# Performance work log

Hardware: AMD Instinct MI355X
Metric: run time of the kernel (lower is better)

The kernel has to match this reference:

```python
import jax, jax.numpy as jnp
import numpy as np

ROUTE_SCALE = 2.5
TOP_K = 2
N_EXPERTS = 16


def setup_inputs() -> dict:
    key = jax.random.key(0)
    ks = jax.random.split(key, 8)
    B, T, D, I, E = 2, 1024, 768, 384, N_EXPERTS
    s = 0.02
    return {
        "x": jax.random.normal(ks[0], (B, T, D), dtype=jnp.float32),
        "gate_w": jax.random.normal(ks[1], (E, D), dtype=jnp.float32) * s,
        "sg_w": jax.random.normal(ks[2], (I, D), dtype=jnp.float32) * s,
        "su_w": jax.random.normal(ks[3], (I, D), dtype=jnp.float32) * s,
        "sd_w": jax.random.normal(ks[4], (D, I), dtype=jnp.float32) * s,
        "rg_w": jax.random.normal(ks[5], (E, I, D), dtype=jnp.float32) * s,
        "ru_w": jax.random.normal(ks[6], (E, I, D), dtype=jnp.float32) * s,
        "rd_w": jax.random.normal(ks[7], (E, D, I), dtype=jnp.float32) * s,
    }


def _moe_forward(x, gate_w, sg_w, su_w, sd_w, rg_w, ru_w, rd_w):
    B, T, D = x.shape
    flat = x.reshape(-1, D)  # (N, D), N = B*T

    # ---- shared expert (SwiGLU FFN) ----
    g = flat @ sg_w.T
    u = flat @ su_w.T
    shared_out = (jax.nn.silu(g) * u) @ sd_w.T  # (N, D)

    # ---- gate: softmax(fp32) -> top-k -> renormalize ----
    logits = (flat @ gate_w.T) * ROUTE_SCALE  # (N, E)
    scores = jax.nn.softmax(logits.astype(jnp.float32), axis=-1)
    topk_w, topk_i = jax.lax.top_k(scores, TOP_K)  # (N, K)
    topk_w = topk_w / jnp.sum(topk_w, axis=-1, keepdims=True)
    topk_w = topk_w.astype(x.dtype)

    # aux load-balancing loss
    one_hot = jax.nn.one_hot(topk_i, N_EXPERTS, dtype=jnp.float32)  # (N, K, E)
    mask = one_hot.sum(axis=1)  # (N, E)
    f = mask.mean(axis=0)
    p = scores.mean(axis=0)
    aux_loss = jnp.sum(f * p) * N_EXPERTS

    # combine weights per (token, expert): sum_k w_k * [idx_k == e]
    combine = jnp.einsum("nk,nke->ne", topk_w, one_hot.astype(x.dtype))  # (N, E)

    # ---- routed experts as batched (grouped) SwiGLU GEMMs ----
    rg = jnp.einsum("nd,eid->nei", flat, rg_w)  # (N, E, I)
    ru = jnp.einsum("nd,eid->nei", flat, ru_w)
    rh = jax.nn.silu(rg) * ru  # (N, E, I)
    eo = jnp.einsum("nei,edi->ned", rh, rd_w)  # (N, E, D)
    routed_out = jnp.einsum("ned,ne->nd", eo, combine)  # (N, D)

    out = (shared_out + routed_out).reshape(B, T, D)
    return out, aux_loss


def reference(x, gate_w, sg_w, su_w, sd_w, rg_w, ru_w, rd_w):
    return _moe_forward(x, gate_w, sg_w, su_w, sd_w, rg_w, ru_w, rd_w)
```

## Files before the change

### kernel.cpp

```cpp
#include <hip/hip_runtime.h>
#include <math.h>

#define NTOK 2048
#define DDIM 768
#define IDIM 384
#define NEXP 16
#define ECAP 2048
#define HSHARED (NEXP * ECAP)
#define GBLK (NTOK / 4)

#define MT 64
#define NSHT2 32
#define NRT2 80
#define NW2 ((NSHT2 + NRT2) * 6)
#define CH2 (NW2 / 8)
#define KH 384

#define ZBLK4 384
#define XBLK4 192
#define W1BLK4 (72 * 17)
#define WDBLK4 (36 * 17)
#define CZBLK (ZBLK4 + XBLK4 + W1BLK4 + WDBLK4)

typedef __attribute__((ext_vector_type(8))) short short8;
typedef __attribute__((ext_vector_type(4))) float f32x4;

__device__ __forceinline__ unsigned short f2bf(float f) {
    unsigned int u = __float_as_uint(f);
    unsigned int r = (u + 0x7fffu + ((u >> 16) & 1u)) >> 16;
    return (unsigned short)r;
}

__device__ __forceinline__ void gload16(const void* g, void* l) {
    __builtin_amdgcn_global_load_lds(
        (const __attribute__((address_space(1))) void*)g,
        (__attribute__((address_space(3))) void*)l, 16, 0, 0);
}

#define WS_XB   1048576u
#define WS_W1F  4194304u
#define WS_WDF  24248320u
#define WS_H    34275328u

__global__ __launch_bounds__(256) void gate_kernel(
    const float* __restrict__ x, const float* __restrict__ gate_w,
    int* __restrict__ topk_i, float* __restrict__ topk_w,
    float* __restrict__ p_partial) {
    __shared__ float p_blk[16];
    int tid = threadIdx.x;
    if (tid < 16) p_blk[tid] = 0.f;
    __syncthreads();

    int wave = tid >> 6, lane = tid & 63;
    int n = blockIdx.x * 4 + wave;
    int e = lane >> 2, q = lane & 3;
    const float4* xr = (const float4*)(x + (size_t)n * DDIM);
    const float4* wr = (const float4*)(gate_w + (size_t)e * DDIM);
    float s = 0.f;
    #pragma unroll 4
    for (int k = q * 48; k < q * 48 + 48; ++k) {
        float4 a = xr[k], b = wr[k];
        s += a.x * b.x + a.y * b.y + a.z * b.z + a.w * b.w;
    }
    s += __shfl_xor(s, 1);
    s += __shfl_xor(s, 2);
    float logit = s * 2.5f;

    float m = logit;
    #pragma unroll
    for (int mask = 4; mask < 64; mask <<= 1)
        m = fmaxf(m, __shfl_xor(m, mask));
    float ex = __expf(logit - m);
    float sum = ex;
    #pragma unroll
    for (int mask = 4; mask < 64; mask <<= 1)
        sum += __shfl_xor(sum, mask);
    float sc = ex / sum;

    float v = sc; int idx = e;
    #pragma unroll
    for (int mask = 4; mask < 64; mask <<= 1) {
        float ov = __shfl_xor(v, mask);
        int   oi = __shfl_xor(idx, mask);
        if (ov > v || (ov == v && oi < idx)) { v = ov; idx = oi; }
    }
    float b0 = v; int i0 = idx;
    v = (e == i0) ? -1.f : sc; idx = e;
    #pragma unroll
    for (int mask = 4; mask < 64; mask <<= 1) {
        float ov = __shfl_xor(v, mask);
        int   oi = __shfl_xor(idx, mask);
        if (ov > v || (ov == v && oi < idx)) { v = ov; idx = oi; }
    }
    float b1 = v; int i1 = idx;
    float rs = 1.f / (b0 + b1);

    if (lane == 0) {
        topk_i[n * 2] = i0; topk_i[n * 2 + 1] = i1;
        topk_w[n * 2] = b0 * rs; topk_w[n * 2 + 1] = b1 * rs;
    }
    if (q == 0) atomicAdd(&p_blk[e], sc);
    __syncthreads();
    if (tid < 16) p_partial[blockIdx.x * 16 + tid] = p_blk[tid];
}

__global__ __launch_bounds__(256) void convzero_kernel(
    const float* __restrict__ x,
    const float* __restrict__ rgw, const float* __restrict__ ruw,
    const float* __restrict__ sgw, const float* __restrict__ suw,
    const float* __restrict__ rdw, const float* __restrict__ sdw,
    float4* __restrict__ out4,
    unsigned short* __restrict__ xb, unsigned short* __restrict__ w1f,
    unsigned short* __restrict__ wdf) {
    int b = blockIdx.x, tid = threadIdx.x;

    if (b < ZBLK4) {
        float4 z = make_float4(0.f, 0.f, 0.f, 0.f);
        float4* dst = out4 + b * 1024 + tid;
        #pragma unroll
        for (int j = 0; j < 4; ++j) dst[j * 256] = z;
        return;
    }
    b -= ZBLK4;

    if (b < XBLK4) {
        #pragma unroll
        for (int j = 0; j < 4; ++j) {
            int i = b * 1024 + j * 256 + tid;
            const float* s = x + (size_t)i * 8;
            float4 v0 = *(const float4*)s, v1 = *(const float4*)(s + 4);
            short8 o;
            o[0]=f2bf(v0.x); o[1]=f2bf(v0.y); o[2]=f2bf(v0.z); o[3]=f2bf(v0.w);
            o[4]=f2bf(v1.x); o[5]=f2bf(v1.y); o[6]=f2bf(v1.z); o[7]=f2bf(v1.w);
            *(short8*)(xb + (size_t)i * 8) = o;
        }
        return;
    }
    b -= XBLK4;

    if (b < W1BLK4) {
        int E = b / 72, bx = b % 72;
        const float* gsrc = (E == 16) ? sgw : rgw + (size_t)E * (IDIM * DDIM);
        const float* usrc = (E == 16) ? suw : ruw + (size_t)E * (IDIM * DDIM);
        unsigned short* wbase = w1f + (size_t)E * (DDIM * DDIM);
        #pragma unroll
        for (int j = 0; j < 4; ++j) {
            int i = bx * 1024 + j * 256 + tid;
            int lane = i & 63;
            int fi = i >> 6;
            int ks = fi % 24, rg = fi / 24;
            int b16 = rg >> 1, gu = rg & 1;
            const float* s = (gu ? usrc : gsrc)
              + (size_t)(b16 * 16 + (lane & 15)) * DDIM + ks * 32 + (lane >> 4) * 8;
            float4 v0 = *(const float4*)s, v1 = *(const float4*)(s + 4);
            short8 o;
            o[0]=f2bf(v0.x); o[1]=f2bf(v0.y); o[2]=f2bf(v0.z); o[3]=f2bf(v0.w);
            o[4]=f2bf(v1.x); o[5]=f2bf(v1.y); o[6]=f2bf(v1.z); o[7]=f2bf(v1.w);
            *(short8*)(wbase + (size_t)i * 8) = o;
        }
        return;
    }
    b -= W1BLK4;

    {
        int E = b / 36, bx = b % 36;
        const float* src = (E == 16) ? sdw : rdw + (size_t)E * (DDIM * IDIM);
        unsigned short* wbase = wdf + (size_t)E * (DDIM * IDIM);
        #pragma unroll
        for (int j = 0; j < 4; ++j) {
            int i = bx * 1024 + j * 256 + tid;
            int lane = i & 63;
            int fi = i >> 6;
            int ks = fi % 12, cg = fi / 12;
            const float* s = src
              + (size_t)(cg * 16 + (lane & 15)) * IDIM + ks * 32 + (lane >> 4) * 8;
            float4 v0 = *(const float4*)s, v1 = *(const float4*)(s + 4);
            short8 o;
            o[0]=f2bf(v0.x); o[1]=f2bf(v0.y); o[2]=f2bf(v0.z); o[3]=f2bf(v0.w);
            o[4]=f2bf(v1.x); o[5]=f2bf(v1.y); o[6]=f2bf(v1.z); o[7]=f2bf(v1.w);
            *(short8*)(wbase + (size_t)i * 8) = o;
        }
    }
}

__global__ __launch_bounds__(256) void route_kernel(
    const int* __restrict__ topk_i, const float* __restrict__ topk_w,
    const float* __restrict__ p_partial,
    int* __restrict__ counts, int* __restrict__ perm_t, float* __restrict__ perm_w,
    float* __restrict__ out_aux) {
    __shared__ float s_p[256];
    __shared__ float s_psum[16];
    __shared__ int s_cnt[16];
    __shared__ int s_cur[16];
    int tid = threadIdx.x;
    {
        int e = tid & 15, g = tid >> 4;
        float acc = 0.f;
        for (int b = g; b < GBLK; b += 16) acc += p_partial[b * 16 + e];
        s_p[tid] = acc;
    }
    if (tid < 16) { s_cnt[tid] = 0; s_cur[tid] = 0; }
    __syncthreads();
    if (tid < 16) {
        float a = 0.f;
        #pragma unroll
        for (int g = 0; g < 16; ++g) a += s_p[g * 16 + tid];
        s_psum[tid] = a;
    }
    for (int n = tid; n < NTOK; n += 256) {
        atomicAdd(&s_cnt[topk_i[n * 2]], 1);
        atomicAdd(&s_cnt[topk_i[n * 2 + 1]], 1);
    }
    __syncthreads();
    if (tid < 16) counts[tid] = s_cnt[tid];
    if (tid == 0) {
        float a = 0.f;
        for (int e = 0; e < 16; ++e) a += (float)s_cnt[e] * s_psum[e];
        out_aux[0] = a * 16.f / ((float)NTOK * (float)NTOK);
    }
    for (int n = tid; n < NTOK; n += 256) {
        #pragma unroll
        for (int k = 0; k < 2; ++k) {
            int e = topk_i[n * 2 + k];
            int pos = atomicAdd(&s_cur[e], 1);
            perm_t[e * ECAP + pos] = n;
            perm_w[e * ECAP + pos] = topk_w[n * 2 + k];
        }
    }
}

__device__ __forceinline__ void swz_decode(int lid, int& bx, int& y) {
    int wid = (lid & 7) * CH2 + (lid >> 3);
    bx = wid / 6;
    y = wid - bx * 6;
}

__device__ __forceinline__ bool tile_decode(const int* __restrict__ counts,
                                            int r, int& e, int& t, int& cnt) {
    int acc = 0;
    for (int ee = 0; ee < NEXP; ++ee) {
        int c = counts[ee];
        int tiles = (c + 63) >> 6;
        if (r < acc + tiles) { e = ee; t = r - acc; cnt = c; return true; }
        acc += tiles;
    }
    return false;
}

__global__ __launch_bounds__(256, 3) void p1_kernel(
    const unsigned short* __restrict__ xb, const unsigned short* __restrict__ w1f,
    const int* __restrict__ counts, const int* __restrict__ perm_t,
    unsigned short* __restrict__ h) {
    __shared__ unsigned short xs[48 * 512];
    __shared__ int s_tok[MT];

    int tid = threadIdx.x;
    int bx, y;
    swz_decode(blockIdx.x, bx, y);
    int e, hbase;
    if (bx < NSHT2) {
        e = 16;
        hbase = HSHARED + bx * MT;
        if (tid < MT) s_tok[tid] = bx * MT + tid;
    } else {
        int t, cnt;
        if (!tile_decode(counts, bx - NSHT2, e, t, cnt)) return;
        hbase = e * ECAP + t * MT;
        if (tid < MT) {
            int slot = t * MT + tid;
            s_tok[tid] = (slot < cnt) ? perm_t[e * ECAP + slot] : 0;
        }
    }
    __syncthreads();

    int lane = tid & 63, wave = tid >> 6;
    int lr = lane & 15, kg8 = (lane >> 4) * 8, jrow = (lane >> 4) * 4;

    const unsigned short* gsrc = xb + (size_t)s_tok[wave * 16 + lr] * DDIM + kg8;

    const unsigned short* pg = w1f + ((((size_t)e * 48 + (y * 8 + wave * 2    )) * 24) * 64 + lane) * 8;
    const unsigned short* pu = w1f + ((((size_t)e * 48 + (y * 8 + wave * 2 + 1)) * 24) * 64 + lane) * 8;

    f32x4 ag0 = (f32x4)0.f, ag1 = (f32x4)0.f, ag2 = (f32x4)0.f, ag3 = (f32x4)0.f;
    f32x4 au0 = (f32x4)0.f, au1 = (f32x4)0.f, au2 = (f32x4)0.f, au3 = (f32x4)0.f;

    #pragma unroll
    for (int half = 0; half < 2; ++half) {
        if (half) __syncthreads();
        #pragma unroll
        for (int c = 0; c < 12; ++c)
            gload16(gsrc + half * KH + c * 32, &xs[(wave * 12 + c) * 512]);
        __syncthreads();

        for (int ks = 0; ks < 12; ++ks) {
            int ksg = half * 12 + ks;
            short8 bg = *(const short8*)(pg + (size_t)ksg * 512);
            short8 bu = *(const short8*)(pu + (size_t)ksg * 512);
            short8 a0 = *(const short8*)(xs + (     ks) * 512 + lane * 8);
            short8 a1 = *(const short8*)(xs + (12 + ks) * 512 + lane * 8);
            short8 a2 = *(const short8*)(xs + (24 + ks) * 512 + lane * 8);
            short8 a3 = *(const short8*)(xs + (36 + ks) * 512 + lane * 8);
            ag0 = __builtin_amdgcn_mfma_f32_16x16x32_bf16(a0, bg, ag0, 0, 0, 0);
            au0 = __builtin_amdgcn_mfma_f32_16x16x32_bf16(a0, bu, au0, 0, 0, 0);
            ag1 = __builtin_amdgcn_mfma_f32_16x16x32_bf16(a1, bg, ag1, 0, 0, 0);
            au1 = __builtin_amdgcn_mfma_f32_16x16x32_bf16(a1, bu, au1, 0, 0, 0);
            ag2 = __builtin_amdgcn_mfma_f32_16x16x32_bf16(a2, bg, ag2, 0, 0, 0);
            au2 = __builtin_amdgcn_mfma_f32_16x16x32_bf16(a2, bu, au2, 0, 0, 0);
            ag3 = __builtin_amdgcn_mfma_f32_16x16x32_bf16(a3, bg, ag3, 0, 0, 0);
            au3 = __builtin_amdgcn_mfma_f32_16x16x32_bf16(a3, bu, au3, 0, 0, 0);
        }
    }

    int colg = y * 64 + wave * 16 + lr;
    #pragma unroll
    for (int mf = 0; mf < 4; ++mf) {
        f32x4 g4 = (mf == 0) ? ag0 : (mf == 1) ? ag1 : (mf == 2) ? ag2 : ag3;
        f32x4 u4 = (mf == 0) ? au0 : (mf == 1) ? au1 : (mf == 2) ? au2 : au3;
        #pragma unroll
        for (int j = 0; j < 4; ++j) {
            int tl = mf * 16 + jrow + j;
            float g = g4[j], u = u4[j];
            float hv = g / (1.f + __expf(-g)) * u;
            h[(size_t)(hbase + tl) * IDIM + colg] = f2bf(hv);
        }
    }
}

__global__ __launch_bounds__(256, 3) void p2_kernel(
    const unsigned short* __restrict__ h, const unsigned short* __restrict__ wdf,
    const int* __restrict__ counts,
    const int* __restrict__ perm_t, const float* __restrict__ perm_w,
    float* __restrict__ out) {
    __shared__ unsigned short hs[48 * 512];
    __shared__ int   s_tok[MT];
    __shared__ float s_w[MT];

    int tid = threadIdx.x;
    int bx, y;
    swz_decode(blockIdx.x, bx, y);
    int e, hbase;
    if (bx < NSHT2) {
        e = 16;
        hbase = HSHARED + bx * MT;
        if (tid < MT) { s_tok[tid] = bx * MT + tid; s_w[tid] = 1.f; }
    } else {
        int t, cnt;
        if (!tile_decode(counts, bx - NSHT2, e, t, cnt)) return;
        hbase = e * ECAP + t * MT;
        if (tid < MT) {
            int slot = t * MT + tid;
            bool v = slot < cnt;
            s_tok[tid] = v ? perm_t[e * ECAP + slot] : 0;
            s_w[tid]   = v ? perm_w[e * ECAP + slot] : 0.f;
        }
    }
    __syncthreads();

    int lane = tid & 63, wave = tid >> 6;
    int lr = lane & 15, kg8 = (lane >> 4) * 8, jrow = (lane >> 4) * 4;

    const unsigned short* gsrc = h + (size_t)(hbase + wave * 16 + lr) * IDIM + kg8;
    #pragma unroll
    for (int c = 0; c < 12; ++c)
        gload16(gsrc + c * 32, &hs[(wave * 12 + c) * 512]);
    __syncthreads();

    const unsigned short* p0 = wdf + ((((size_t)e * 48 + (y * 8 + wave * 2    )) * 12) * 64 + lane) * 8;
    const unsigned short* p1 = wdf + ((((size_t)e * 48 + (y * 8 + wave * 2 + 1)) * 12) * 64 + lane) * 8;

    f32x4 c00 = (f32x4)0.f, c01 = (f32x4)0.f, c02 = (f32x4)0.f, c03 = (f32x4)0.f;
    f32x4 c10 = (f32x4)0.f, c11 = (f32x4)0.f, c12 = (f32x4)0.f, c13 = (f32x4)0.f;
    for (int ks = 0; ks < 12; ++ks) {
        short8 b0 = *(const short8*)(p0 + (size_t)ks * 512);
        short8 b1 = *(const short8*)(p1 + (size_t)ks * 512);
        short8 a0 = *(const short8*)(hs + (     ks) * 512 + lane * 8);
        short8 a1 = *(const short8*)(hs + (12 + ks) * 512 + lane * 8);
        short8 a2 = *(const short8*)(hs + (24 + ks) * 512 + lane * 8);
        short8 a3 = *(const short8*)(hs + (36 + ks) * 512 + lane * 8);
        c00 = __builtin_amdgcn_mfma_f32_16x16x32_bf16(a0, b0, c00, 0, 0, 0);
        c10 = __builtin_amdgcn_mfma_f32_16x16x32_bf16(a0, b1, c10, 0, 0, 0);
        c01 = __builtin_amdgcn_mfma_f32_16x16x32_bf16(a1, b0, c01, 0, 0, 0);
        c11 = __builtin_amdgcn_mfma_f32_16x16x32_bf16(a1, b1, c11, 0, 0, 0);
        c02 = __builtin_amdgcn_mfma_f32_16x16x32_bf16(a2, b0, c02, 0, 0, 0);
        c12 = __builtin_amdgcn_mfma_f32_16x16x32_bf16(a2, b1, c12, 0, 0, 0);
        c03 = __builtin_amdgcn_mfma_f32_16x16x32_bf16(a3, b0, c03, 0, 0, 0);
        c13 = __builtin_amdgcn_mfma_f32_16x16x32_bf16(a3, b1, c13, 0, 0, 0);
    }

    int col0 = y * 128 + wave * 32 + lr;
    #pragma unroll
    for (int mf = 0; mf < 4; ++mf) {
        f32x4 v0 = (mf == 0) ? c00 : (mf == 1) ? c01 : (mf == 2) ? c02 : c03;
        f32x4 v1 = (mf == 0) ? c10 : (mf == 1) ? c11 : (mf == 2) ? c12 : c13;
        #pragma unroll
        for (int j = 0; j < 4; ++j) {
            int tl = mf * 16 + jrow + j;
            float w = s_w[tl];
            if (w == 0.f) continue;
            float* orow = out + (size_t)s_tok[tl] * DDIM;
            atomicAdd(orow + col0,      w * v0[j]);
            atomicAdd(orow + col0 + 16, w * v1[j]);
        }
    }
}

extern "C" void kernel_launch(void* const* d_in, const int* in_sizes, int n_in,
                              void* d_out, int out_size, void* d_ws, size_t ws_size,
                              hipStream_t stream) {
    const float* x      = (const float*)d_in[0];
    const float* gate_w = (const float*)d_in[1];
    const float* sg_w   = (const float*)d_in[2];
    const float* su_w   = (const float*)d_in[3];
    const float* sd_w   = (const float*)d_in[4];
    const float* rg_w   = (const float*)d_in[5];
    const float* ru_w   = (const float*)d_in[6];
    const float* rd_w   = (const float*)d_in[7];
    float* out = (float*)d_out;

    char* ws = (char*)d_ws;
    int*   counts    = (int*)(ws + 0);
    int*   perm_t    = (int*)(ws + 1024);
    float* perm_w    = (float*)(ws + 132096);
    float* p_partial = (float*)(ws + 263168);
    int*   topk_i    = (int*)(ws + 295936);
    float* topk_w    = (float*)(ws + 312320);
    unsigned short* xb  = (unsigned short*)(ws + WS_XB);
    unsigned short* w1f = (unsigned short*)(ws + WS_W1F);
    unsigned short* wdf = (unsigned short*)(ws + WS_WDF);
    unsigned short* hbuf= (unsigned short*)(ws + WS_H);

    gate_kernel<<<GBLK, 256, 0, stream>>>(x, gate_w, topk_i, topk_w, p_partial);

    convzero_kernel<<<CZBLK, 256, 0, stream>>>(
        x, rg_w, ru_w, sg_w, su_w, rd_w, sd_w,
        (float4*)out, xb, w1f, wdf);

    route_kernel<<<1, 256, 0, stream>>>(topk_i, topk_w, p_partial,
                                        counts, perm_t, perm_w,
                                        out + (size_t)NTOK * DDIM);

    p1_kernel<<<NW2, 256, 0, stream>>>(xb, w1f, counts, perm_t, hbuf);

    p2_kernel<<<NW2, 256, 0, stream>>>(hbuf, wdf, counts, perm_t, perm_w, out);
}
```

Measured before the change: 101.8 us.

## Fuse routing into conversion kernel, stage weight repack via LDS, shrink GEMM LDS chunks

Merges the single-block route kernel into the conversion/zeroing kernel as block 0, removing one launch and its serialization. Weight repacking to the MFMA fragment layout now reads rows coalesced into a padded LDS buffer and writes fragments out, instead of doing strided scattered global reads. The p1 and p2 GEMM kernels load their activation tile in smaller K chunks, halving LDS use so occupancy can rise from 3 to 4 blocks per CU, at the cost of more barriers.

```diff
diff --git a/kernel.cpp b/kernel.cpp
--- a/kernel.cpp
+++ b/kernel.cpp
@@ -14,13 +14,12 @@
 #define NRT2 80
 #define NW2 ((NSHT2 + NRT2) * 6)
 #define CH2 (NW2 / 8)
-#define KH 384
-
-#define ZBLK4 384
-#define XBLK4 192
-#define W1BLK4 (72 * 17)
-#define WDBLK4 (36 * 17)
-#define CZBLK (ZBLK4 + XBLK4 + W1BLK4 + WDBLK4)
+
+#define CR_Z0 1
+#define CR_X0 (CR_Z0 + 384)
+#define CR_W10 (CR_X0 + 192)
+#define CR_WD0 (CR_W10 + 816)
+#define CR_END (CR_WD0 + 816)
 
 typedef __attribute__((ext_vector_type(8))) short short8;
 typedef __attribute__((ext_vector_type(4))) float f32x4;
@@ -104,29 +103,76 @@
     if (tid < 16) p_partial[blockIdx.x * 16 + tid] = p_blk[tid];
 }
 
-__global__ __launch_bounds__(256) void convzero_kernel(
+__global__ __launch_bounds__(256) void convroute_kernel(
     const float* __restrict__ x,
     const float* __restrict__ rgw, const float* __restrict__ ruw,
     const float* __restrict__ sgw, const float* __restrict__ suw,
     const float* __restrict__ rdw, const float* __restrict__ sdw,
     float4* __restrict__ out4,
     unsigned short* __restrict__ xb, unsigned short* __restrict__ w1f,
-    unsigned short* __restrict__ wdf) {
+    unsigned short* __restrict__ wdf,
+    const int* __restrict__ topk_i, const float* __restrict__ topk_w,
+    const float* __restrict__ p_partial,
+    int* __restrict__ counts, int* __restrict__ perm_t, float* __restrict__ perm_w,
+    float* __restrict__ out_aux) {
+    __shared__ unsigned short sbuf[16 * 780];
     int b = blockIdx.x, tid = threadIdx.x;
 
-    if (b < ZBLK4) {
+    if (b == 0) {
+        float* s_p    = (float*)sbuf;
+        float* s_psum = s_p + 256;
+        int*   s_cnt  = (int*)(s_psum + 16);
+        int*   s_cur  = s_cnt + 16;
+        {
+            int e = tid & 15, g = tid >> 4;
+            float acc = 0.f;
+            for (int bb = g; bb < GBLK; bb += 16) acc += p_partial[bb * 16 + e];
+            s_p[tid] = acc;
+        }
+        if (tid < 16) { s_cnt[tid] = 0; s_cur[tid] = 0; }
+        __syncthreads();
+        if (tid < 16) {
+            float a = 0.f;
+            #pragma unroll
+            for (int g = 0; g < 16; ++g) a += s_p[g * 16 + tid];
+            s_psum[tid] = a;
+        }
+        for (int n = tid; n < NTOK; n += 256) {
+            atomicAdd(&s_cnt[topk_i[n * 2]], 1);
+            atomicAdd(&s_cnt[topk_i[n * 2 + 1]], 1);
+        }
+        __syncthreads();
+        if (tid < 16) counts[tid] = s_cnt[tid];
+        if (tid == 0) {
+            float a = 0.f;
+            for (int e = 0; e < 16; ++e) a += (float)s_cnt[e] * s_psum[e];
+            out_aux[0] = a * 16.f / ((float)NTOK * (float)NTOK);
+        }
+        for (int n = tid; n < NTOK; n += 256) {
+            #pragma unroll
+            for (int k = 0; k < 2; ++k) {
+                int e = topk_i[n * 2 + k];
+                int pos = atomicAdd(&s_cur[e], 1);
+                perm_t[e * ECAP + pos] = n;
+                perm_w[e * ECAP + pos] = topk_w[n * 2 + k];
+            }
+        }
+        return;
+    }
+
+    if (b < CR_X0) {
         float4 z = make_float4(0.f, 0.f, 0.f, 0.f);
-        float4* dst = out4 + b * 1024 + tid;
+        float4* dst = out4 + (b - CR_Z0) * 1024 + tid;
         #pragma unroll
         for (int j = 0; j < 4; ++j) dst[j * 256] = z;
         return;
     }
-    b -= ZBLK4;
-
-    if (b < XBLK4) {
+
+    if (b < CR_W10) {
+        int bb = b - CR_X0;
         #pragma unroll
         for (int j = 0; j < 4; ++j) {
-            int i = b * 1024 + j * 256 + tid;
+            int i = bb * 1024 + j * 256 + tid;
             const float* s = x + (size_t)i * 8;
             float4 v0 = *(const float4*)s, v1 = *(const float4*)(s + 4);
             short8 o;
@@ -136,95 +182,56 @@
         }
         return;
     }
-    b -= XBLK4;
-
-    if (b < W1BLK4) {
-        int E = b / 72, bx = b % 72;
-        const float* gsrc = (E == 16) ? sgw : rgw + (size_t)E * (IDIM * DDIM);
-        const float* usrc = (E == 16) ? suw : ruw + (size_t)E * (IDIM * DDIM);
-        unsigned short* wbase = w1f + (size_t)E * (DDIM * DDIM);
-        #pragma unroll
-        for (int j = 0; j < 4; ++j) {
-            int i = bx * 1024 + j * 256 + tid;
-            int lane = i & 63;
-            int fi = i >> 6;
-            int ks = fi % 24, rg = fi / 24;
-            int b16 = rg >> 1, gu = rg & 1;
-            const float* s = (gu ? usrc : gsrc)
-              + (size_t)(b16 * 16 + (lane & 15)) * DDIM + ks * 32 + (lane >> 4) * 8;
-            float4 v0 = *(const float4*)s, v1 = *(const float4*)(s + 4);
-            short8 o;
-            o[0]=f2bf(v0.x); o[1]=f2bf(v0.y); o[2]=f2bf(v0.z); o[3]=f2bf(v0.w);
-            o[4]=f2bf(v1.x); o[5]=f2bf(v1.y); o[6]=f2bf(v1.z); o[7]=f2bf(v1.w);
-            *(short8*)(wbase + (size_t)i * 8) = o;
+
+    if (b < CR_WD0) {
+        int bb = b - CR_W10;
+        int E = bb / 48, rg = bb % 48;
+        const float* gsrc_ = (E == 16) ? sgw : rgw + (size_t)E * (IDIM * DDIM);
+        const float* usrc_ = (E == 16) ? suw : ruw + (size_t)E * (IDIM * DDIM);
+        const float* src = ((rg & 1) ? usrc_ : gsrc_) + (size_t)(rg >> 1) * 16 * DDIM;
+        #pragma unroll
+        for (int i = 0; i < 12; ++i) {
+            int idx = i * 256 + tid;
+            int r = idx / 192, c4 = idx - r * 192;
+            float4 v = ((const float4*)(src + (size_t)r * DDIM))[c4];
+            ushort4 o4;
+            o4.x = f2bf(v.x); o4.y = f2bf(v.y); o4.z = f2bf(v.z); o4.w = f2bf(v.w);
+            *(ushort4*)(sbuf + r * 780 + c4 * 4) = o4;
+        }
+        __syncthreads();
+        unsigned short* wbase = w1f + (size_t)E * (DDIM * DDIM) + (size_t)rg * 24 * 512;
+        #pragma unroll
+        for (int c = 0; c < 6; ++c) {
+            int cc = c * 256 + tid;
+            int ks = cc >> 6, l = cc & 63;
+            short8 v8 = *(const short8*)(sbuf + (l & 15) * 780 + ks * 32 + (l >> 4) * 8);
+            *(short8*)(wbase + (size_t)(ks * 64 + l) * 8) = v8;
         }
         return;
     }
-    b -= W1BLK4;
 
     {
-        int E = b / 36, bx = b % 36;
-        const float* src = (E == 16) ? sdw : rdw + (size_t)E * (DDIM * IDIM);
-        unsigned short* wbase = wdf + (size_t)E * (DDIM * IDIM);
-        #pragma unroll
-        for (int j = 0; j < 4; ++j) {
-            int i = bx * 1024 + j * 256 + tid;
-            int lane = i & 63;
-            int fi = i >> 6;
-            int ks = fi % 12, cg = fi / 12;
-            const float* s = src
-              + (size_t)(cg * 16 + (lane & 15)) * IDIM + ks * 32 + (lane >> 4) * 8;
-            float4 v0 = *(const float4*)s, v1 = *(const float4*)(s + 4);
-            short8 o;
-            o[0]=f2bf(v0.x); o[1]=f2bf(v0.y); o[2]=f2bf(v0.z); o[3]=f2bf(v0.w);
-            o[4]=f2bf(v1.x); o[5]=f2bf(v1.y); o[6]=f2bf(v1.z); o[7]=f2bf(v1.w);
-            *(short8*)(wbase + (size_t)i * 8) = o;
-        }
-    }
-}
-
-__global__ __launch_bounds__(256) void route_kernel(
-    const int* __restrict__ topk_i, const float* __restrict__ topk_w,
-    const float* __restrict__ p_partial,
-    int* __restrict__ counts, int* __restrict__ perm_t, float* __restrict__ perm_w,
-    float* __restrict__ out_aux) {
-    __shared__ float s_p[256];
-    __shared__ float s_psum[16];
-    __shared__ int s_cnt[16];
-    __shared__ int s_cur[16];
-    int tid = threadIdx.x;
-    {
-        int e = tid & 15, g = tid >> 4;
-        float acc = 0.f;
-        for (int b = g; b < GBLK; b += 16) acc += p_partial[b * 16 + e];
-        s_p[tid] = acc;
-    }
-    if (tid < 16) { s_cnt[tid] = 0; s_cur[tid] = 0; }
-    __syncthreads();
-    if (tid < 16) {
-        float a = 0.f;
-        #pragma unroll
-        for (int g = 0; g < 16; ++g) a += s_p[g * 16 + tid];
-        s_psum[tid] = a;
-    }
-    for (int n = tid; n < NTOK; n += 256) {
-        atomicAdd(&s_cnt[topk_i[n * 2]], 1);
-        atomicAdd(&s_cnt[topk_i[n * 2 + 1]], 1);
-    }
-    __syncthreads();
-    if (tid < 16) counts[tid] = s_cnt[tid];
-    if (tid == 0) {
-        float a = 0.f;
-        for (int e = 0; e < 16; ++e) a += (float)s_cnt[e] * s_psum[e];
-        out_aux[0] = a * 16.f / ((float)NTOK * (float)NTOK);
-    }
-    for (int n = tid; n < NTOK; n += 256) {
-        #pragma unroll
-        for (int k = 0; k < 2; ++k) {
-            int e = topk_i[n * 2 + k];
-            int pos = atomicAdd(&s_cur[e], 1);
-            perm_t[e * ECAP + pos] = n;
-            perm_w[e * ECAP + pos] = topk_w[n * 2 + k];
+        int bb = b - CR_WD0;
+        int E = bb / 48, cg = bb % 48;
+        const float* src = ((E == 16) ? sdw : rdw + (size_t)E * (DDIM * IDIM))
+                         + (size_t)cg * 16 * IDIM;
+        #pragma unroll
+        for (int i = 0; i < 6; ++i) {
+            int idx = i * 256 + tid;
+            int r = idx / 96, c4 = idx - r * 96;
+            float4 v = ((const float4*)(src + (size_t)r * IDIM))[c4];
+            ushort4 o4;
+            o4.x = f2bf(v.x); o4.y = f2bf(v.y); o4.z = f2bf(v.z); o4.w = f2bf(v.w);
+            *(ushort4*)(sbuf + r * 390 + c4 * 4) = o4;
+        }
+        __syncthreads();
+        unsigned short* wbase = wdf + (size_t)E * (DDIM * IDIM) + (size_t)cg * 12 * 512;
+        #pragma unroll
+        for (int c = 0; c < 3; ++c) {
+            int cc = c * 256 + tid;
+            int ks = cc >> 6, l = cc & 63;
+            short8 v8 = *(const short8*)(sbuf + (l & 15) * 390 + ks * 32 + (l >> 4) * 8);
+            *(short8*)(wbase + (size_t)(ks * 64 + l) * 8) = v8;
         }
     }
 }
@@ -247,11 +254,11 @@
     return false;
 }
 
-__global__ __launch_bounds__(256, 3) void p1_kernel(
+__global__ __launch_bounds__(256, 4) void p1_kernel(
     const unsigned short* __restrict__ xb, const unsigned short* __restrict__ w1f,
     const int* __restrict__ counts, const int* __restrict__ perm_t,
     unsigned short* __restrict__ h) {
-    __shared__ unsigned short xs[48 * 512];
+    __shared__ unsigned short xs[24 * 512];
     __shared__ int s_tok[MT];
 
     int tid = threadIdx.x;
@@ -284,22 +291,22 @@
     f32x4 ag0 = (f32x4)0.f, ag1 = (f32x4)0.f, ag2 = (f32x4)0.f, ag3 = (f32x4)0.f;
     f32x4 au0 = (f32x4)0.f, au1 = (f32x4)0.f, au2 = (f32x4)0.f, au3 = (f32x4)0.f;
 
-    #pragma unroll
-    for (int half = 0; half < 2; ++half) {
-        if (half) __syncthreads();
-        #pragma unroll
-        for (int c = 0; c < 12; ++c)
-            gload16(gsrc + half * KH + c * 32, &xs[(wave * 12 + c) * 512]);
-        __syncthreads();
-
-        for (int ks = 0; ks < 12; ++ks) {
-            int ksg = half * 12 + ks;
+    for (int ch = 0; ch < 4; ++ch) {
+        if (ch) __syncthreads();
+        #pragma unroll
+        for (int c = 0; c < 6; ++c)
+            gload16(gsrc + (ch * 6 + c) * 32, &xs[(wave * 6 + c) * 512]);
+        __syncthreads();
+
+        #pragma unroll
+        for (int ksl = 0; ksl < 6; ++ksl) {
+            int ksg = ch * 6 + ksl;
             short8 bg = *(const short8*)(pg + (size_t)ksg * 512);
             short8 bu = *(const short8*)(pu + (size_t)ksg * 512);
-            short8 a0 = *(const short8*)(xs + (     ks) * 512 + lane * 8);
-            short8 a1 = *(const short8*)(xs + (12 + ks) * 512 + lane * 8);
-            short8 a2 = *(const short8*)(xs + (24 + ks) * 512 + lane * 8);
-            short8 a3 = *(const short8*)(xs + (36 + ks) * 512 + lane * 8);
+            short8 a0 = *(const short8*)(xs + (     ksl) * 512 + lane * 8);
+            short8 a1 = *(const short8*)(xs + ( 6 + ksl) * 512 + lane * 8);
+            short8 a2 = *(const short8*)(xs + (12 + ksl) * 512 + lane * 8);
+            short8 a3 = *(const short8*)(xs + (18 + ksl) * 512 + lane * 8);
             ag0 = __builtin_amdgcn_mfma_f32_16x16x32_bf16(a0, bg, ag0, 0, 0, 0);
             au0 = __builtin_amdgcn_mfma_f32_16x16x32_bf16(a0, bu, au0, 0, 0, 0);
             ag1 = __builtin_amdgcn_mfma_f32_16x16x32_bf16(a1, bg, ag1, 0, 0, 0);
@@ -326,12 +333,12 @@
     }
 }
 
-__global__ __launch_bounds__(256, 3) void p2_kernel(
+__global__ __launch_bounds__(256, 4) void p2_kernel(
     const unsigned short* __restrict__ h, const unsigned short* __restrict__ wdf,
     const int* __restrict__ counts,
     const int* __restrict__ perm_t, const float* __restrict__ perm_w,
     float* __restrict__ out) {
-    __shared__ unsigned short hs[48 * 512];
+    __shared__ unsigned short hs[24 * 512];
     __shared__ int   s_tok[MT];
     __shared__ float s_w[MT];
 
@@ -360,31 +367,38 @@
     int lr = lane & 15, kg8 = (lane >> 4) * 8, jrow = (lane >> 4) * 4;
 
     const unsigned short* gsrc = h + (size_t)(hbase + wave * 16 + lr) * IDIM + kg8;
-    #pragma unroll
-    for (int c = 0; c < 12; ++c)
-        gload16(gsrc + c * 32, &hs[(wave * 12 + c) * 512]);
-    __syncthreads();
 
     const unsigned short* p0 = wdf + ((((size_t)e * 48 + (y * 8 + wave * 2    )) * 12) * 64 + lane) * 8;
     const unsigned short* p1 = wdf + ((((size_t)e * 48 + (y * 8 + wave * 2 + 1)) * 12) * 64 + lane) * 8;
 
     f32x4 c00 = (f32x4)0.f, c01 = (f32x4)0.f, c02 = (f32x4)0.f, c03 = (f32x4)0.f;
     f32x4 c10 = (f32x4)0.f, c11 = (f32x4)0.f, c12 = (f32x4)0.f, c13 = (f32x4)0.f;
-    for (int ks = 0; ks < 12; ++ks) {
-        short8 b0 = *(const short8*)(p0 + (size_t)ks * 512);
-        short8 b1 = *(const short8*)(p1 + (size_t)ks * 512);
-        short8 a0 = *(const short8*)(hs + (     ks) * 512 + lane * 8);
-        short8 a1 = *(const short8*)(hs + (12 + ks) * 512 + lane * 8);
-        short8 a2 = *(const short8*)(hs + (24 + ks) * 512 + lane * 8);
-        short8 a3 = *(const short8*)(hs + (36 + ks) * 512 + lane * 8);
-        c00 = __builtin_amdgcn_mfma_f32_16x16x32_bf16(a0, b0, c00, 0, 0, 0);
-        c10 = __builtin_amdgcn_mfma_f32_16x16x32_bf16(a0, b1, c10, 0, 0, 0);
-        c01 = __builtin_amdgcn_mfma_f32_16x16x32_bf16(a1, b0, c01, 0, 0, 0);
-        c11 = __builtin_amdgcn_mfma_f32_16x16x32_bf16(a1, b1, c11, 0, 0, 0);
-        c02 = __builtin_amdgcn_mfma_f32_16x16x32_bf16(a2, b0, c02, 0, 0, 0);
-        c12 = __builtin_amdgcn_mfma_f32_16x16x32_bf16(a2, b1, c12, 0, 0, 0);
-        c03 = __builtin_amdgcn_mfma_f32_16x16x32_bf16(a3, b0, c03, 0, 0, 0);
-        c13 = __builtin_amdgcn_mfma_f32_16x16x32_bf16(a3, b1, c13, 0, 0, 0);
+
+    for (int ch = 0; ch < 2; ++ch) {
+        if (ch) __syncthreads();
+        #pragma unroll
+        for (int c = 0; c < 6; ++c)
+            gload16(gsrc + (ch * 6 + c) * 32, &hs[(wave * 6 + c) * 512]);
+        __syncthreads();
+
+        #pragma unroll
+        for (int ksl = 0; ksl < 6; ++ksl) {
+            int ksg = ch * 6 + ksl;
+            short8 b0 = *(const short8*)(p0 + (size_t)ksg * 512);
+            short8 b1 = *(const short8*)(p1 + (size_t)ksg * 512);
+            short8 a0 = *(const short8*)(hs + (     ksl) * 512 + lane * 8);
+            short8 a1 = *(const short8*)(hs + ( 6 + ksl) * 512 + lane * 8);
+            short8 a2 = *(const short8*)(hs + (12 + ksl) * 512 + lane * 8);
+            short8 a3 = *(const short8*)(hs + (18 + ksl) * 512 + lane * 8);
+            c00 = __builtin_amdgcn_mfma_f32_16x16x32_bf16(a0, b0, c00, 0, 0, 0);
+            c10 = __builtin_amdgcn_mfma_f32_16x16x32_bf16(a0, b1, c10, 0, 0, 0);
+            c01 = __builtin_amdgcn_mfma_f32_16x16x32_bf16(a1, b0, c01, 0, 0, 0);
+            c11 = __builtin_amdgcn_mfma_f32_16x16x32_bf16(a1, b1, c11, 0, 0, 0);
+            c02 = __builtin_amdgcn_mfma_f32_16x16x32_bf16(a2, b0, c02, 0, 0, 0);
+            c12 = __builtin_amdgcn_mfma_f32_16x16x32_bf16(a2, b1, c12, 0, 0, 0);
+            c03 = __builtin_amdgcn_mfma_f32_16x16x32_bf16(a3, b0, c03, 0, 0, 0);
+            c13 = __builtin_amdgcn_mfma_f32_16x16x32_bf16(a3, b1, c13, 0, 0, 0);
+        }
     }
 
     int col0 = y * 128 + wave * 32 + lr;
@@ -431,13 +445,11 @@
 
     gate_kernel<<<GBLK, 256, 0, stream>>>(x, gate_w, topk_i, topk_w, p_partial);
 
-    convzero_kernel<<<CZBLK, 256, 0, stream>>>(
+    convroute_kernel<<<CR_END, 256, 0, stream>>>(
         x, rg_w, ru_w, sg_w, su_w, rd_w, sd_w,
-        (float4*)out, xb, w1f, wdf);
-
-    route_kernel<<<1, 256, 0, stream>>>(topk_i, topk_w, p_partial,
-                                        counts, perm_t, perm_w,
-                                        out + (size_t)NTOK * DDIM);
+        (float4*)out, xb, w1f, wdf,
+        topk_i, topk_w, p_partial, counts, perm_t, perm_w,
+        out + (size_t)NTOK * DDIM);
 
     p1_kernel<<<NW2, 256, 0, stream>>>(xb, w1f, counts, perm_t, hbuf);
 
```

Measured after the change: 97.37 us. 1.05x faster.
